# Kernel optimization log

Hardware: AMD Instinct MI355X
Metric: run time of the kernel (lower is better)

Reference implementation:

```python
import jax, jax.numpy as jnp
import numpy as np

B, L, D_MODEL = 2, 2048, 1024
D_INNER, D_STATE, DT_RANK, D_CONV = 2048, 16, 64, 4
EPS = 1e-5


def setup_inputs() -> dict:
    key = jax.random.key(0)
    ks = jax.random.split(key, 12)
    s = lambda fan: 1.0 / np.sqrt(fan)
    return {
        "x": jax.random.normal(ks[0], (B, L, D_MODEL), jnp.float32),
        "norm_w": jnp.ones((D_MODEL,), jnp.float32),
        "W_in": jax.random.normal(ks[1], (2 * D_INNER, D_MODEL), jnp.float32) * s(D_MODEL),
        "W_conv": jax.random.normal(ks[2], (D_INNER, D_CONV), jnp.float32) * s(D_CONV),
        "b_conv": jnp.zeros((D_INNER,), jnp.float32),
        "W_xproj": jax.random.normal(ks[3], (DT_RANK + 2 * D_STATE, D_INNER), jnp.float32) * s(D_INNER),
        "W_dt": jax.random.normal(ks[4], (D_INNER, DT_RANK), jnp.float32) * s(DT_RANK),
        "b_dt": jax.random.normal(ks[5], (D_INNER,), jnp.float32) * 0.1,
        # A initialized as log(1..d_state) per channel (standard Mamba S4D-real init)
        "A_log": jnp.log(jnp.broadcast_to(jnp.arange(1, D_STATE + 1, dtype=jnp.float32), (D_INNER, D_STATE))),
        "D": jnp.ones((D_INNER,), jnp.float32),
        "W_out": jax.random.normal(ks[6], (D_MODEL, D_INNER), jnp.float32) * s(D_INNER),
    }


def _mamba_residual(x, norm_w, W_in, W_conv, b_conv, W_xproj, W_dt, b_dt, A_log, D, W_out):
    # RMSNorm
    xn = x * jax.lax.rsqrt(jnp.mean(x * x, axis=-1, keepdims=True) + EPS) * norm_w
    # in_proj -> split into u (ssm branch) and z (gate)
    xz = jnp.einsum("bld,ed->ble", xn, W_in)            # [b, l, 2*d_inner]
    u, z = jnp.split(xz, 2, axis=-1)                     # each [b, l, d_inner]
    # depthwise causal conv1d over time
    u_t = jnp.transpose(u, (0, 2, 1))                    # [b, d_inner, l]
    u_c = jax.lax.conv_general_dilated(
        u_t, W_conv[:, None, :], window_strides=(1,),
        padding=[(D_CONV - 1, 0)], feature_group_count=D_INNER,
        dimension_numbers=("NCH", "OIH", "NCH"))
    u_c = jax.nn.silu(u_c + b_conv[None, :, None])       # [b, d_inner, l]
    u = jnp.transpose(u_c, (0, 2, 1))                    # [b, l, d_inner]
    # x_proj -> (dt, B, C)
    x_dbl = jnp.einsum("bld,ed->ble", u, W_xproj)        # [b, l, dt_rank+2n]
    dt, Bm, Cm = jnp.split(x_dbl, [DT_RANK, DT_RANK + D_STATE], axis=-1)
    dt = jax.nn.softplus(jnp.einsum("blr,dr->bld", dt, W_dt) + b_dt)  # [b, l, d_inner]
    A = -jnp.exp(A_log)                                  # [d_inner, n]

    # selective scan over time
    def step(h, ins):
        dt_t, B_t, C_t, u_t = ins                        # [b,d],[b,n],[b,n],[b,d]
        dA = jnp.exp(dt_t[..., None] * A)                # [b, d, n]
        h = dA * h + (dt_t * u_t)[..., None] * B_t[:, None, :]
        y = jnp.einsum("bdn,bn->bd", h, C_t)
        return h, y

    h0 = jnp.zeros((x.shape[0], D_INNER, D_STATE), x.dtype)
    ins = (jnp.transpose(dt, (1, 0, 2)), jnp.transpose(Bm, (1, 0, 2)),
           jnp.transpose(Cm, (1, 0, 2)), jnp.transpose(u, (1, 0, 2)))
    _, ys = jax.lax.scan(step, h0, ins)                  # [l, b, d_inner]
    y = jnp.transpose(ys, (1, 0, 2)) + u * D             # [b, l, d_inner]
    y = y * jax.nn.silu(z)
    out = jnp.einsum("ble,de->bld", y, W_out)
    return out + x  # residual (block_mode 'residual'/'none')


def reference(x, norm_w, W_in, W_conv, b_conv, W_xproj, W_dt, b_dt, A_log, D, W_out):
    return _mamba_residual(x, norm_w, W_in, W_conv, b_conv, W_xproj, W_dt, b_dt, A_log, D, W_out)
```

## Files before the change

kernel.cpp:

```cpp
#include <hip/hip_runtime.h>

typedef unsigned short u16;
typedef unsigned int u32;
typedef short bf16x8 __attribute__((ext_vector_type(8)));
typedef float f32x4 __attribute__((ext_vector_type(4)));

static constexpr int LS = 2048;
static constexpr int DM = 1024;
static constexpr int DI = 2048;
static constexpr int DSn = 16;
static constexpr int DTRk = 64;
static constexpr int MR = 4096;
static constexpr int NCH = 64;
static constexpr int CL = LS / NCH;
static constexpr float L2E = 1.44269504f;

#define DEV __device__ __forceinline__

DEV u16 f2bf(float f) {
  u32 u = __float_as_uint(f);
  u32 r = (u + 0x7FFF + ((u >> 16) & 1)) >> 16;
  return (u16)r;
}
DEV float bf2f(u16 h) { return __uint_as_float(((u32)h) << 16); }

DEV void gload16(const u16* g, u16* l) {
  __builtin_amdgcn_global_load_lds((const __attribute__((address_space(1))) u32*)g,
                                   (__attribute__((address_space(3))) u32*)l, 16, 0, 0);
}

DEV void bar() { asm volatile("s_barrier" ::: "memory"); }
DEV void wait_lgkm0() {
  asm volatile("s_waitcnt lgkmcnt(0)" ::: "memory");
  __builtin_amdgcn_sched_barrier(0);
}

#define CALC_POWERS(dst, basev)                                              \
  do {                                                                       \
    const float e1_ = (basev);                                               \
    const float e2_ = e1_ * e1_, e3_ = e2_ * e1_, e4_ = e2_ * e2_;           \
    const float e5_ = e4_ * e1_, e6_ = e4_ * e2_, e7_ = e4_ * e3_,           \
                e8_ = e4_ * e4_;                                             \
    dst[0] = e1_; dst[1] = e2_; dst[2] = e3_; dst[3] = e4_;                  \
    dst[4] = e5_; dst[5] = e6_; dst[6] = e7_; dst[7] = e8_;                  \
    dst[8] = e8_ * e1_;  dst[9] = e8_ * e2_;  dst[10] = e8_ * e3_;           \
    dst[11] = e8_ * e4_; dst[12] = e8_ * e5_; dst[13] = e8_ * e6_;           \
    dst[14] = e8_ * e7_; dst[15] = e8_ * e8_;                                \
  } while (0)

__global__ __launch_bounds__(256) void cvt_weights(const float* __restrict__ W_in,
                                                   const float* __restrict__ W_out,
                                                   const float* __restrict__ W_dt,
                                                   const float* __restrict__ W_xp,
                                                   u16* __restrict__ Win_b,
                                                   u16* __restrict__ Wout_b,
                                                   u16* __restrict__ Wdt_b,
                                                   u16* __restrict__ Wxp_b) {
  const int N0 = 4096 * 1024;
  const int N1 = N0 + 1024 * 2048;
  const int N2 = N1 + 2048 * 64;
  const int N3 = N2 + 128 * 2048;
  int i = blockIdx.x * 256 + threadIdx.x;
  const int stride = gridDim.x * 256;
  for (; i < N3; i += stride) {
    if (i < N0) {
      Win_b[i] = f2bf(W_in[i]);
    } else if (i < N1) {
      const int j = i - N0; Wout_b[j] = f2bf(W_out[j]);
    } else if (i < N2) {
      const int j = i - N1; Wdt_b[j] = f2bf(W_dt[j]);
    } else {
      const int j = i - N2; const int r = j >> 11, c = j & 2047;
      Wxp_b[j] = (r < 96) ? f2bf(W_xp[r * 2048 + c]) : (u16)0;
    }
  }
}

__global__ __launch_bounds__(256) void rmsnorm_kernel(const float* __restrict__ x,
                                                      const float* __restrict__ w,
                                                      u16* __restrict__ xn) {
  const int row = blockIdx.x;
  const int tid = threadIdx.x;
  const float4 v = reinterpret_cast<const float4*>(x + (size_t)row * DM)[tid];
  float ss = v.x * v.x + v.y * v.y + v.z * v.z + v.w * v.w;
#pragma unroll
  for (int o = 32; o; o >>= 1) ss += __shfl_xor(ss, o);
  __shared__ float red[4];
  if ((tid & 63) == 0) red[tid >> 6] = ss;
  __syncthreads();
  const float tot = red[0] + red[1] + red[2] + red[3];
  const float scale = rsqrtf(tot * (1.0f / DM) + 1e-5f);
  const float4 wv = reinterpret_cast<const float4*>(w)[tid];
  ushort4 o4;
  o4.x = f2bf(v.x * scale * wv.x);
  o4.y = f2bf(v.y * scale * wv.y);
  o4.z = f2bf(v.z * scale * wv.z);
  o4.w = f2bf(v.w * scale * wv.w);
  *reinterpret_cast<ushort4*>(&xn[(size_t)row * DM + tid * 4]) = o4;
}

DEV void stage_op(const u16* __restrict__ P, int K, int rowbase, int k0,
                  u16* dst, int tid) {
#pragma unroll
  for (int i = 0; i < 4; ++i) {
    const int row = i * 64 + (tid >> 3);
    const int slot = (tid & 7) ^ (row & 7);
    gload16(P + (size_t)(rowbase + row) * K + k0 + slot * 8, dst + i * 4096 + tid * 8);
  }
}

#define LOAD_A(MH) do { \
  _Pragma("unroll") for (int m_ = 0; m_ < 4; ++m_) \
  _Pragma("unroll") for (int kk_ = 0; kk_ < 2; ++kk_) \
    a[m_][kk_] = *reinterpret_cast<const bf16x8*>( \
        &Asl[curo + wr * 8192 + ((MH) * 64 + m_ * 16 + lrow) * 64 + ((kk_ * 4 + kq) ^ rsw) * 8]); \
} while (0)

#define LOAD_B(NH) do { \
  _Pragma("unroll") for (int n_ = 0; n_ < 2; ++n_) \
  _Pragma("unroll") for (int kk_ = 0; kk_ < 2; ++kk_) \
    b[(NH) * 2 + n_][kk_] = *reinterpret_cast<const bf16x8*>( \
        &Bsl[curo + bh * 8192 + (bq * 64 + ((NH) * 2 + n_) * 16 + lrow) * 64 + ((kk_ * 4 + kq) ^ rsw) * 8]); \
} while (0)

#define MMA_QUAD(MH, NH) do { \
  _Pragma("unroll") for (int m_ = 0; m_ < 4; ++m_) \
  _Pragma("unroll") for (int n_ = 0; n_ < 2; ++n_) \
  _Pragma("unroll") for (int kk_ = 0; kk_ < 2; ++kk_) \
    acc[(MH) * 4 + m_][(NH) * 2 + n_] = __builtin_amdgcn_mfma_f32_16x16x32_bf16( \
        a[m_][kk_], b[(NH) * 2 + n_][kk_], acc[(MH) * 4 + m_][(NH) * 2 + n_], 0, 0, 0); \
} while (0)

__global__ __launch_bounds__(512, 2) void gemm256_bf16(const u16* __restrict__ A,
                                                       const u16* __restrict__ Bw,
                                                       int M, int N, int K,
                                                       u16* __restrict__ outB) {
  __shared__ __align__(16) u16 Asl[2 * 16384];
  __shared__ __align__(16) u16 Bsl[2 * 16384];
  const int tid = threadIdx.x;
  const int lane = tid & 63;
  const int wid = tid >> 6;
  const int wr = wid >> 2;
  const int wc = wid & 3;
  const int lrow = lane & 15;
  const int kq = lane >> 4;
  const int rsw = lane & 7;
  const int bh = wc >> 1, bq = wc & 1;

  const int nwg = gridDim.x * gridDim.y;
  int wg = blockIdx.y * gridDim.x + blockIdx.x;
  wg = (wg & 7) * (nwg >> 3) + (wg >> 3);
  const int bn = (wg % gridDim.x) * 256;
  const int bm = (wg / gridDim.x) * 256;

  const int nt = K >> 6;

  f32x4 acc[8][4] = {};
  bf16x8 a[4][2], b[4][2];

  stage_op(A, K, bm, 0, &Asl[0], tid);
  stage_op(Bw, K, bn, 0, &Bsl[0], tid);
  stage_op(A, K, bm, 64, &Asl[16384], tid);
  stage_op(Bw, K, bn, 64, &Bsl[16384], tid);
  asm volatile("s_waitcnt vmcnt(8)" ::: "memory");
  __builtin_amdgcn_sched_barrier(0);
  bar();

  for (int t = 0; t < nt; ++t) {
    const int curo = (t & 1) * 16384;
    LOAD_A(0); LOAD_B(0);
    bar(); wait_lgkm0();
    __builtin_amdgcn_s_setprio(1); MMA_QUAD(0, 0); __builtin_amdgcn_s_setprio(0);
    bar();
    LOAD_B(1);
    bar(); wait_lgkm0();
    __builtin_amdgcn_s_setprio(1); MMA_QUAD(0, 1); __builtin_amdgcn_s_setprio(0);
    bar();
    LOAD_A(1);
    if (t < nt - 2) stage_op(Bw, K, bn, (t + 2) * 64, &Bsl[curo], tid);
    bar(); wait_lgkm0();
    __builtin_amdgcn_s_setprio(1); MMA_QUAD(1, 0); __builtin_amdgcn_s_setprio(0);
    bar();
    if (t < nt - 2) stage_op(A, K, bm, (t + 2) * 64, &Asl[curo], tid);
    bar();
    __builtin_amdgcn_s_setprio(1); MMA_QUAD(1, 1); __builtin_amdgcn_s_setprio(0);
    if (t == nt - 2) { asm volatile("s_waitcnt vmcnt(0)" ::: "memory"); }
    else if (t < nt - 2) { asm volatile("s_waitcnt vmcnt(6)" ::: "memory"); }
    bar();
  }

#pragma unroll
  for (int m = 0; m < 8; ++m)
#pragma unroll
    for (int n = 0; n < 4; ++n) {
      const int col = bn + wc * 64 + n * 16 + lrow;
#pragma unroll
      for (int rr = 0; rr < 4; ++rr) {
        const int row = bm + wr * 128 + m * 16 + kq * 4 + rr;
        outB[(size_t)row * N + col] = f2bf(acc[m][n][rr]);
      }
    }
}

template <int EPI>
__global__ __launch_bounds__(256) void gemm_bt(const u16* __restrict__ A,
                                               const u16* __restrict__ Bw,
                                               int M, int N, int K, int Klen,
                                               float* __restrict__ outF,
                                               u16* __restrict__ outB,
                                               const float* __restrict__ aux) {
  __shared__ __align__(16) u16 As[128 * 32];
  __shared__ __align__(16) u16 Bs[128 * 32];
  const int tid = threadIdx.x;
  const int lane = tid & 63;
  const int wid = tid >> 6;
  const int wr = wid >> 1, wc = wid & 1;
  const int nwg = gridDim.x * gridDim.y;
  int wg = blockIdx.y * gridDim.x + blockIdx.x;
  wg = (wg & 7) * (nwg >> 3) + (wg >> 3);
  const int bn = (wg % gridDim.x) * 128;
  const int bm = (wg / gridDim.x) * 128;
  const int koff = blockIdx.z * Klen;
  const int r0 = tid >> 2;
  const int c0 = (tid & 3) * 8;
  const int lrow = lane & 15, kq = lane >> 4;

  f32x4 acc[4][4] = {};

  const u16* Ab = A + (size_t)bm * K + koff;
  const u16* Bb = Bw + (size_t)bn * K + koff;

  for (int k0 = 0; k0 < Klen; k0 += 32) {
    gload16(Ab + (size_t)r0 * K + k0 + c0, &As[r0 * 32 + c0]);
    gload16(Ab + (size_t)(r0 + 64) * K + k0 + c0, &As[(r0 + 64) * 32 + c0]);
    gload16(Bb + (size_t)r0 * K + k0 + c0, &Bs[r0 * 32 + c0]);
    gload16(Bb + (size_t)(r0 + 64) * K + k0 + c0, &Bs[(r0 + 64) * 32 + c0]);
    __syncthreads();
    bf16x8 af[4], bfr[4];
#pragma unroll
    for (int m = 0; m < 4; ++m)
      af[m] = *reinterpret_cast<const bf16x8*>(&As[(wr * 64 + m * 16 + lrow) * 32 + kq * 8]);
#pragma unroll
    for (int n = 0; n < 4; ++n)
      bfr[n] = *reinterpret_cast<const bf16x8*>(&Bs[(wc * 64 + n * 16 + lrow) * 32 + kq * 8]);
#pragma unroll
    for (int m = 0; m < 4; ++m)
#pragma unroll
      for (int n = 0; n < 4; ++n)
        acc[m][n] = __builtin_amdgcn_mfma_f32_16x16x32_bf16(af[m], bfr[n], acc[m][n], 0, 0, 0);
    __syncthreads();
  }

  float* dstF = (EPI == 4) ? outF + (size_t)blockIdx.z * MR * N : outF;
#pragma unroll
  for (int m = 0; m < 4; ++m) {
#pragma unroll
    for (int n = 0; n < 4; ++n) {
      const int col = bn + wc * 64 + n * 16 + lrow;
#pragma unroll
      for (int r = 0; r < 4; ++r) {
        const int row = bm + wr * 64 + m * 16 + kq * 4 + r;
        const float v = acc[m][n][r];
        if (EPI == 2) {
          const float xv = v + aux[col];
          const float sp = fmaxf(xv, 0.f) + log1pf(__expf(-fabsf(xv)));
          outB[(size_t)row * N + col] = f2bf(sp);
        } else {
          dstF[(size_t)row * N + col] = v;
        }
      }
    }
  }
}

__global__ __launch_bounds__(256) void outproj_reduce(const float* __restrict__ p,
                                                      const float* __restrict__ x,
                                                      float* __restrict__ out) {
  const int id = blockIdx.x * 256 + threadIdx.x;
  const float4 a = reinterpret_cast<const float4*>(p)[id];
  const float4 b = reinterpret_cast<const float4*>(p + (size_t)MR * 1024)[id];
  const float4 c = reinterpret_cast<const float4*>(x)[id];
  float4 o;
  o.x = a.x + b.x + c.x;
  o.y = a.y + b.y + c.y;
  o.z = a.z + b.z + c.z;
  o.w = a.w + b.w + c.w;
  reinterpret_cast<float4*>(out)[id] = o;
}

__global__ __launch_bounds__(256) void gemm_xproj_splitk(const u16* __restrict__ A,
                                                         const u16* __restrict__ Bw,
                                                         float* __restrict__ p0,
                                                         float* __restrict__ p1) {
  __shared__ __align__(16) u16 As[128 * 32];
  __shared__ __align__(16) u16 Bs[128 * 32];
  const int tid = threadIdx.x;
  const int lane = tid & 63;
  const int wid = tid >> 6;
  const int wr = wid >> 1, wc = wid & 1;
  const int kp = blockIdx.x;
  const int bm = blockIdx.y * 128;
  const int koff = kp * 256;
  const int r0 = tid >> 2;
  const int c0 = (tid & 3) * 8;
  const int lrow = lane & 15, kq = lane >> 4;

  f32x4 acc[4][4] = {};
  const u16* Ab = A + (size_t)bm * DI + koff;
  const u16* Bb = Bw + koff;

  for (int k0 = 0; k0 < 256; k0 += 32) {
    gload16(Ab + (size_t)r0 * DI + k0 + c0, &As[r0 * 32 + c0]);
    gload16(Ab + (size_t)(r0 + 64) * DI + k0 + c0, &As[(r0 + 64) * 32 + c0]);
    gload16(Bb + (size_t)r0 * DI + k0 + c0, &Bs[r0 * 32 + c0]);
    gload16(Bb + (size_t)(r0 + 64) * DI + k0 + c0, &Bs[(r0 + 64) * 32 + c0]);
    __syncthreads();
    bf16x8 af[4], bfr[4];
#pragma unroll
    for (int m = 0; m < 4; ++m)
      af[m] = *reinterpret_cast<const bf16x8*>(&As[(wr * 64 + m * 16 + lrow) * 32 + kq * 8]);
#pragma unroll
    for (int n = 0; n < 4; ++n)
      bfr[n] = *reinterpret_cast<const bf16x8*>(&Bs[(wc * 64 + n * 16 + lrow) * 32 + kq * 8]);
#pragma unroll
    for (int m = 0; m < 4; ++m)
#pragma unroll
      for (int n = 0; n < 4; ++n)
        acc[m][n] = __builtin_amdgcn_mfma_f32_16x16x32_bf16(af[m], bfr[n], acc[m][n], 0, 0, 0);
    __syncthreads();
  }

  float* dst = (kp < 4 ? p0 : p1) + (size_t)(kp & 3) * MR * 128;
#pragma unroll
  for (int m = 0; m < 4; ++m)
#pragma unroll
    for (int n = 0; n < 4; ++n) {
      const int col = wc * 64 + n * 16 + lrow;
#pragma unroll
      for (int r = 0; r < 4; ++r) {
        const int row = bm + wr * 64 + m * 16 + kq * 4 + r;
        dst[(size_t)row * 128 + col] = acc[m][n][r];
      }
    }
}

__global__ __launch_bounds__(256) void xproj_reduce(const float* __restrict__ p0,
                                                    const float* __restrict__ p1,
                                                    float* __restrict__ xdbl,
                                                    u16* __restrict__ dtr) {
  const int id = blockIdx.x * 256 + threadIdx.x;
  const int row = id >> 7, col = id & 127;
  float s = 0.f;
#pragma unroll
  for (int kp = 0; kp < 4; ++kp) s += p0[(size_t)kp * MR * 128 + id];
#pragma unroll
  for (int kp = 0; kp < 4; ++kp) s += p1[(size_t)kp * MR * 128 + id];
  if (col < 96) xdbl[(size_t)row * 96 + col] = s;
  if (col < 64) dtr[(size_t)row * 64 + col] = f2bf(s);
}

__global__ __launch_bounds__(256) void conv_silu_kernel(const u16* __restrict__ xz,
                                                        const float* __restrict__ Wc,
                                                        const float* __restrict__ bc,
                                                        u16* __restrict__ uc) {
  const int id = blockIdx.x * 256 + threadIdx.x;
  const int d8 = id & (DI / 8 - 1);
  const int t = (id >> 8) & (LS - 1);
  const int b = id >> 19;
  const int d0 = d8 * 8;
  const size_t rowb = (size_t)b * LS;
  bf16x8 r[4];
#pragma unroll
  for (int k = 0; k < 4; ++k) {
    const int tt = t - 3 + k;
    if (tt >= 0)
      r[k] = *reinterpret_cast<const bf16x8*>(&xz[(rowb + tt) * (2 * DI) + d0]);
    else
      r[k] = bf16x8{0, 0, 0, 0, 0, 0, 0, 0};
  }
  const float4 bc0 = *reinterpret_cast<const float4*>(&bc[d0]);
  const float4 bc1 = *reinterpret_cast<const float4*>(&bc[d0 + 4]);
  const float bcv[8] = {bc0.x, bc0.y, bc0.z, bc0.w, bc1.x, bc1.y, bc1.z, bc1.w};
  u16 o[8];
#pragma unroll
  for (int j = 0; j < 8; ++j) {
    const float4 w = *reinterpret_cast<const float4*>(&Wc[(d0 + j) * 4]);
    float s = bcv[j];
    s += bf2f((u16)r[0][j]) * w.x;
    s += bf2f((u16)r[1][j]) * w.y;
    s += bf2f((u16)r[2][j]) * w.z;
    s += bf2f((u16)r[3][j]) * w.w;
    const float sl = s / (1.f + __expf(-s));
    o[j] = f2bf(sl);
  }
  *reinterpret_cast<bf16x8*>(&uc[(rowb + t) * DI + d0]) =
      *reinterpret_cast<const bf16x8*>(o);
}


__global__ __launch_bounds__(128, 4) void scan_phase1(const u16* __restrict__ dtb,
                                                      const float* __restrict__ xdbl,
                                                      const u16* __restrict__ uc,
                                                      const float* __restrict__ Alog,
                                                      float* __restrict__ P,
                                                      float* __restrict__ S) {
  __shared__ __align__(16) u16 s_dt[16 * 128];
  __shared__ __align__(16) u16 s_uc[16 * 128];
  __shared__ __align__(16) float s_b[16 * 16];
  const int tid = threadIdx.x;
  const int blk = blockIdx.x;
  const int d0 = (blk & 15) * 128;
  const int c = (blk >> 4) & (NCH - 1);
  const int b = blk >> 10;
  const int d = d0 + tid;
  const size_t tbase = (size_t)b * LS + c * CL;

  float Av[16];
  bool fastA = true;
#pragma unroll
  for (int j = 0; j < 16; j += 4) {
    const float4 Alv = *reinterpret_cast<const float4*>(&Alog[d * DSn + j]);
    Av[j + 0] = -__expf(Alv.x); Av[j + 1] = -__expf(Alv.y);
    Av[j + 2] = -__expf(Alv.z); Av[j + 3] = -__expf(Alv.w);
  }
#pragma unroll
  for (int j = 0; j < 16; ++j)
    fastA = fastA && (fabsf(Av[j] + (float)(j + 1)) < 1e-3f * (float)(j + 1));

  float h[16];
#pragma unroll
  for (int j = 0; j < 16; ++j) h[j] = 0.f;
  float sdt = 0.f;

  for (int w = 0; w < 2; ++w) {
    const size_t twb = tbase + w * 16;
#pragma unroll
    for (int j = 0; j < 2; ++j) {
      const int k = j * 128 + tid;
      const int row = k >> 4, col = (k & 15) * 8;
      gload16(dtb + (twb + row) * DI + d0 + col, &s_dt[row * 128 + col]);
      gload16(uc + (twb + row) * DI + d0 + col, &s_uc[row * 128 + col]);
    }
    if (tid < 64) {
      gload16((const u16*)(xdbl + (twb + (tid >> 2)) * 96 + DTRk + (tid & 3) * 4),
              (u16*)&s_b[tid * 4]);
    }
    __syncthreads();
    if (fastA) {
      for (int tr = 0; tr < 16; ++tr) {
        const float dtv = bf2f(s_dt[tr * 128 + tid]);
        const float uv = bf2f(s_uc[tr * 128 + tid]);
        const float du = dtv * uv;
        sdt += dtv;
        float dA[16];
        CALC_POWERS(dA, exp2f(-L2E * dtv));
        float Bf[16];
#pragma unroll
        for (int j = 0; j < 16; j += 4) {
          const float4 Bv = *reinterpret_cast<const float4*>(&s_b[tr * 16 + j]);
          Bf[j] = Bv.x; Bf[j + 1] = Bv.y; Bf[j + 2] = Bv.z; Bf[j + 3] = Bv.w;
        }
#pragma unroll
        for (int j = 0; j < 16; ++j) h[j] = dA[j] * h[j] + du * Bf[j];
      }
    } else {
      for (int tr = 0; tr < 16; ++tr) {
        const float dtv = bf2f(s_dt[tr * 128 + tid]);
        const float uv = bf2f(s_uc[tr * 128 + tid]);
        const float du = dtv * uv;
        sdt += dtv;
        float Bf[16];
#pragma unroll
        for (int j = 0; j < 16; j += 4) {
          const float4 Bv = *reinterpret_cast<const float4*>(&s_b[tr * 16 + j]);
          Bf[j] = Bv.x; Bf[j + 1] = Bv.y; Bf[j + 2] = Bv.z; Bf[j + 3] = Bv.w;
        }
#pragma unroll
        for (int j = 0; j < 16; ++j)
          h[j] = exp2f(dtv * Av[j] * L2E) * h[j] + du * Bf[j];
      }
    }
    __syncthreads();
  }

  const size_t oi = (((size_t)b * NCH + c) * DI + d) * DSn;
  float Pw[16];
  if (fastA) {
    CALC_POWERS(Pw, exp2f(-L2E * sdt));
  } else {
#pragma unroll
    for (int j = 0; j < 16; ++j) Pw[j] = exp2f(Av[j] * L2E * sdt);
  }
#pragma unroll
  for (int j = 0; j < 16; j += 4) {
    float4 Sv = {h[j], h[j + 1], h[j + 2], h[j + 3]};
    float4 Pv = {Pw[j], Pw[j + 1], Pw[j + 2], Pw[j + 3]};
    *reinterpret_cast<float4*>(&S[oi + j]) = Sv;
    *reinterpret_cast<float4*>(&P[oi + j]) = Pv;
  }
}

__global__ __launch_bounds__(256) void scan_phase2(const float* __restrict__ P,
                                                   float* __restrict__ S) {
  const int gid = blockIdx.x * 256 + threadIdx.x;
  const int ng = gid & 3;
  const int d = (gid >> 2) & (DI - 1);
  const int b = gid >> 13;
  float4 h = {0.f, 0.f, 0.f, 0.f};
  for (int cc = 0; cc < NCH; ++cc) {
    const size_t oi = (((size_t)b * NCH + cc) * DI + d) * DSn + ng * 4;
    const float4 Pv = *reinterpret_cast<const float4*>(&P[oi]);
    const float4 Sv = *reinterpret_cast<const float4*>(&S[oi]);
    *reinterpret_cast<float4*>(&S[oi]) = h;
    h.x = Sv.x + Pv.x * h.x;
    h.y = Sv.y + Pv.y * h.y;
    h.z = Sv.z + Pv.z * h.z;
    h.w = Sv.w + Pv.w * h.w;
  }
}

__global__ __launch_bounds__(128, 4) void scan_phase3(const u16* __restrict__ dtb,
                                                      const float* __restrict__ xdbl,
                                                      const u16* __restrict__ uc,
                                                      const u16* __restrict__ xz,
                                                      const float* __restrict__ Alog,
                                                      const float* __restrict__ Dp,
                                                      const float* __restrict__ Hin,
                                                      u16* __restrict__ yb) {
  __shared__ __align__(16) u16 s_dt[16 * 128];
  __shared__ __align__(16) u16 s_uc[16 * 128];
  __shared__ __align__(16) u16 s_z[16 * 128];
  __shared__ __align__(16) float s_bc[16 * 32];
  const int tid = threadIdx.x;
  const int blk = blockIdx.x;
  const int d0 = (blk & 15) * 128;
  const int c = (blk >> 4) & (NCH - 1);
  const int b = blk >> 10;
  const int d = d0 + tid;
  const size_t tbase = (size_t)b * LS + c * CL;

  float Av[16];
  bool fastA = true;
#pragma unroll
  for (int j = 0; j < 16; j += 4) {
    const float4 Alv = *reinterpret_cast<const float4*>(&Alog[d * DSn + j]);
    Av[j + 0] = -__expf(Alv.x); Av[j + 1] = -__expf(Alv.y);
    Av[j + 2] = -__expf(Alv.z); Av[j + 3] = -__expf(Alv.w);
  }
#pragma unroll
  for (int j = 0; j < 16; ++j)
    fastA = fastA && (fabsf(Av[j] + (float)(j + 1)) < 1e-3f * (float)(j + 1));

  const float Dd = Dp[d];
  const size_t oi = (((size_t)b * NCH + c) * DI + d) * DSn;
  float h[16];
#pragma unroll
  for (int j = 0; j < 16; j += 4) {
    const float4 hv = *reinterpret_cast<const float4*>(&Hin[oi + j]);
    h[j] = hv.x; h[j + 1] = hv.y; h[j + 2] = hv.z; h[j + 3] = hv.w;
  }

  for (int w = 0; w < 2; ++w) {
    const size_t twb = tbase + w * 16;
#pragma unroll
    for (int j = 0; j < 2; ++j) {
      const int k = j * 128 + tid;
      const int row = k >> 4, col = (k & 15) * 8;
      gload16(dtb + (twb + row) * DI + d0 + col, &s_dt[row * 128 + col]);
      gload16(uc + (twb + row) * DI + d0 + col, &s_uc[row * 128 + col]);
      gload16(xz + (twb + row) * (2 * DI) + DI + d0 + col, &s_z[row * 128 + col]);
    }
    {
      gload16((const u16*)(xdbl + (twb + (tid >> 3)) * 96 + DTRk + (tid & 7) * 4),
              (u16*)&s_bc[tid * 4]);
    }
    __syncthreads();
#define P3_STEP(DA_STMT)                                                        \
    for (int tr = 0; tr < 16; ++tr) {                                           \
      const float dtv = bf2f(s_dt[tr * 128 + tid]);                             \
      const float uv = bf2f(s_uc[tr * 128 + tid]);                              \
      const float du = dtv * uv;                                                \
      float dA[16];                                                             \
      DA_STMT;                                                                  \
      float Bf[16], Cf[16];                                                     \
      _Pragma("unroll")                                                         \
      for (int j = 0; j < 16; j += 4) {                                         \
        const float4 Bv = *reinterpret_cast<const float4*>(&s_bc[tr * 32 + j]); \
        const float4 Cv = *reinterpret_cast<const float4*>(&s_bc[tr * 32 + 16 + j]); \
        Bf[j] = Bv.x; Bf[j + 1] = Bv.y; Bf[j + 2] = Bv.z; Bf[j + 3] = Bv.w;     \
        Cf[j] = Cv.x; Cf[j + 1] = Cv.y; Cf[j + 2] = Cv.z; Cf[j + 3] = Cv.w;     \
      }                                                                         \
      _Pragma("unroll")                                                         \
      for (int j = 0; j < 16; ++j) h[j] = dA[j] * h[j] + du * Bf[j];            \
      float y0 = 0.f, y1 = 0.f, y2 = 0.f, y3 = 0.f;                             \
      _Pragma("unroll")                                                         \
      for (int j = 0; j < 16; j += 4) {                                         \
        y0 += h[j] * Cf[j];                                                     \
        y1 += h[j + 1] * Cf[j + 1];                                             \
        y2 += h[j + 2] * Cf[j + 2];                                             \
        y3 += h[j + 3] * Cf[j + 3];                                             \
      }                                                                         \
      const float y = (y0 + y1) + (y2 + y3) + uv * Dd;                          \
      const float z = bf2f(s_z[tr * 128 + tid]);                                \
      const float sz = z / (1.f + __expf(-z));                                  \
      yb[(twb + tr) * DI + d] = f2bf(y * sz);                                   \
    }
    if (fastA) {
      P3_STEP(CALC_POWERS(dA, exp2f(-L2E * dtv)));
    } else {
      P3_STEP({ _Pragma("unroll") for (int j = 0; j < 16; ++j) dA[j] = exp2f(dtv * Av[j] * L2E); });
    }
#undef P3_STEP
    __syncthreads();
  }
}

extern "C" void kernel_launch(void* const* d_in, const int* in_sizes, int n_in,
                              void* d_out, int out_size, void* d_ws, size_t ws_size,
                              hipStream_t stream) {
  (void)in_sizes; (void)n_in; (void)out_size; (void)ws_size;
  const float* x      = (const float*)d_in[0];
  const float* norm_w = (const float*)d_in[1];
  const float* W_in   = (const float*)d_in[2];
  const float* W_conv = (const float*)d_in[3];
  const float* b_conv = (const float*)d_in[4];
  const float* W_xp   = (const float*)d_in[5];
  const float* W_dt   = (const float*)d_in[6];
  const float* b_dt   = (const float*)d_in[7];
  const float* A_log  = (const float*)d_in[8];
  const float* Dvec   = (const float*)d_in[9];
  const float* W_out  = (const float*)d_in[10];
  float* out = (float*)d_out;

  char* ws = (char*)d_ws;
  size_t off = 0;
  auto alloc = [&](size_t bytes) -> void* {
    void* p = ws + off;
    off += (bytes + 255) & ~(size_t)255;
    return p;
  };
  u16* Win_b  = (u16*)alloc((size_t)4096 * 1024 * 2);
  u16* Wout_b = (u16*)alloc((size_t)1024 * 2048 * 2);
  u16* Wxp_b  = (u16*)alloc((size_t)128 * 2048 * 2);
  u16* Wdt_b  = (u16*)alloc((size_t)2048 * 64 * 2);
  u16* xn_b   = (u16*)alloc((size_t)MR * DM * 2);
  u16* xz_b   = (u16*)alloc((size_t)MR * 2 * DI * 2);
  u16* uc_b   = (u16*)alloc((size_t)MR * DI * 2);
  float* xdbl = (float*)alloc((size_t)MR * 96 * 4);
  u16* dtr_b  = (u16*)alloc((size_t)MR * 64 * 2);
  u16* dtf_b  = (u16*)alloc((size_t)MR * DI * 2);
  u16* y_b    = (u16*)alloc((size_t)MR * DI * 2);
  float* Sbuf = (float*)alloc((size_t)2 * NCH * DI * DSn * 4);
  float* part0 = (float*)Win_b;
  float* part1 = (float*)xn_b;
  float* Pbuf = (float*)y_b;
  float* opart = (float*)xz_b;

  cvt_weights<<<2048, 256, 0, stream>>>(W_in, W_out, W_dt, W_xp,
                                        Win_b, Wout_b, Wdt_b, Wxp_b);

  rmsnorm_kernel<<<MR, 256, 0, stream>>>(x, norm_w, xn_b);

  gemm256_bf16<<<dim3(16, 16), 512, 0, stream>>>(xn_b, Win_b, MR, 4096, 1024, xz_b);
  conv_silu_kernel<<<4096, 256, 0, stream>>>(xz_b, W_conv, b_conv, uc_b);
  gemm_xproj_splitk<<<dim3(8, 32), 256, 0, stream>>>(uc_b, Wxp_b, part0, part1);
  xproj_reduce<<<2048, 256, 0, stream>>>(part0, part1, xdbl, dtr_b);
  gemm_bt<2><<<dim3(16, 32), 256, 0, stream>>>(dtr_b, Wdt_b, MR, 2048, 64, 64,
                                               nullptr, dtf_b, b_dt);
  scan_phase1<<<2048, 128, 0, stream>>>(dtf_b, xdbl, uc_b, A_log, Pbuf, Sbuf);
  scan_phase2<<<64, 256, 0, stream>>>(Pbuf, Sbuf);
  scan_phase3<<<2048, 128, 0, stream>>>(dtf_b, xdbl, uc_b, xz_b, A_log, Dvec,
                                        Sbuf, y_b);
  gemm_bt<4><<<dim3(8, 32, 2), 256, 0, stream>>>(y_b, Wout_b, MR, 1024, 2048, 1024,
                                                 opart, nullptr, nullptr);
  outproj_reduce<<<4096, 256, 0, stream>>>(opart, x, out);
}
```

Baseline: 231.3 us.

## Run out-projection on pipelined 256x256 GEMM with 4-way split-K

```diff
diff --git a/kernel.cpp b/kernel.cpp
--- a/kernel.cpp
+++ b/kernel.cpp
@@ -131,10 +131,12 @@
         a[m_][kk_], b[(NH) * 2 + n_][kk_], acc[(MH) * 4 + m_][(NH) * 2 + n_], 0, 0, 0); \
 } while (0)
 
-__global__ __launch_bounds__(512, 2) void gemm256_bf16(const u16* __restrict__ A,
-                                                       const u16* __restrict__ Bw,
-                                                       int M, int N, int K,
-                                                       u16* __restrict__ outB) {
+template <int EPI>
+__global__ __launch_bounds__(512, 2) void gemm256(const u16* __restrict__ A,
+                                                  const u16* __restrict__ Bw,
+                                                  int M, int N, int K, int Klen,
+                                                  u16* __restrict__ outB,
+                                                  float* __restrict__ outF) {
   __shared__ __align__(16) u16 Asl[2 * 16384];
   __shared__ __align__(16) u16 Bsl[2 * 16384];
   const int tid = threadIdx.x;
@@ -152,16 +154,17 @@
   wg = (wg & 7) * (nwg >> 3) + (wg >> 3);
   const int bn = (wg % gridDim.x) * 256;
   const int bm = (wg / gridDim.x) * 256;
-
-  const int nt = K >> 6;
+  const int koff = blockIdx.z * Klen;
+
+  const int nt = Klen >> 6;
 
   f32x4 acc[8][4] = {};
   bf16x8 a[4][2], b[4][2];
 
-  stage_op(A, K, bm, 0, &Asl[0], tid);
-  stage_op(Bw, K, bn, 0, &Bsl[0], tid);
-  stage_op(A, K, bm, 64, &Asl[16384], tid);
-  stage_op(Bw, K, bn, 64, &Bsl[16384], tid);
+  stage_op(A, K, bm, koff, &Asl[0], tid);
+  stage_op(Bw, K, bn, koff, &Bsl[0], tid);
+  stage_op(A, K, bm, koff + 64, &Asl[16384], tid);
+  stage_op(Bw, K, bn, koff + 64, &Bsl[16384], tid);
   asm volatile("s_waitcnt vmcnt(8)" ::: "memory");
   __builtin_amdgcn_sched_barrier(0);
   bar();
@@ -177,36 +180,62 @@
     __builtin_amdgcn_s_setprio(1); MMA_QUAD(0, 1); __builtin_amdgcn_s_setprio(0);
     bar();
     LOAD_A(1);
-    if (t < nt - 2) stage_op(Bw, K, bn, (t + 2) * 64, &Bsl[curo], tid);
+    if (t < nt - 2) stage_op(Bw, K, bn, koff + (t + 2) * 64, &Bsl[curo], tid);
     bar(); wait_lgkm0();
     __builtin_amdgcn_s_setprio(1); MMA_QUAD(1, 0); __builtin_amdgcn_s_setprio(0);
     bar();
-    if (t < nt - 2) stage_op(A, K, bm, (t + 2) * 64, &Asl[curo], tid);
+    if (t < nt - 2) stage_op(A, K, bm, koff + (t + 2) * 64, &Asl[curo], tid);
     bar();
     __builtin_amdgcn_s_setprio(1); MMA_QUAD(1, 1); __builtin_amdgcn_s_setprio(0);
     if (t == nt - 2) { asm volatile("s_waitcnt vmcnt(0)" ::: "memory"); }
-    else if (t < nt - 2) { asm volatile("s_waitcnt vmcnt(6)" ::: "memory"); }
+    else if (t < nt - 2) { asm volatile("s_waitcnt vmcnt(8)" ::: "memory"); }
     bar();
   }
 
-#pragma unroll
-  for (int m = 0; m < 8; ++m)
-#pragma unroll
-    for (int n = 0; n < 4; ++n) {
-      const int col = bn + wc * 64 + n * 16 + lrow;
-#pragma unroll
-      for (int rr = 0; rr < 4; ++rr) {
-        const int row = bm + wr * 128 + m * 16 + kq * 4 + rr;
-        outB[(size_t)row * N + col] = f2bf(acc[m][n][rr]);
+  if (EPI == 0) {
+#pragma unroll
+    for (int m = 0; m < 8; ++m)
+#pragma unroll
+      for (int n = 0; n < 4; ++n) {
+        const int col = bn + wc * 64 + n * 16 + lrow;
+#pragma unroll
+        for (int rr = 0; rr < 4; ++rr) {
+          const int row = bm + wr * 128 + m * 16 + kq * 4 + rr;
+          outB[(size_t)row * N + col] = f2bf(acc[m][n][rr]);
+        }
       }
-    }
-}
-
-template <int EPI>
-__global__ __launch_bounds__(256) void gemm_bt(const u16* __restrict__ A,
+  } else {
+    float* dstF = outF + (size_t)blockIdx.z * MR * N;
+#pragma unroll
+    for (int m = 0; m < 8; ++m)
+#pragma unroll
+      for (int n = 0; n < 4; ++n) {
+        const int col = bn + wc * 64 + n * 16 + lrow;
+#pragma unroll
+        for (int rr = 0; rr < 4; ++rr) {
+          const int row = bm + wr * 128 + m * 16 + kq * 4 + rr;
+          dstF[(size_t)row * N + col] = acc[m][n][rr];
+        }
+      }
+  }
+}
+
+__global__ __launch_bounds__(256) void outproj_reduce4(const float* __restrict__ p,
+                                                       const float* __restrict__ x,
+                                                       float* __restrict__ out) {
+  const int id = blockIdx.x * 256 + threadIdx.x;
+  float4 o = reinterpret_cast<const float4*>(x)[id];
+#pragma unroll
+  for (int s = 0; s < 4; ++s) {
+    const float4 a = reinterpret_cast<const float4*>(p + (size_t)s * MR * 1024)[id];
+    o.x += a.x; o.y += a.y; o.z += a.z; o.w += a.w;
+  }
+  reinterpret_cast<float4*>(out)[id] = o;
+}
+
+__global__ __launch_bounds__(256) void gemm_dt(const u16* __restrict__ A,
                                                const u16* __restrict__ Bw,
-                                               int M, int N, int K, int Klen,
-                                               float* __restrict__ outF,
+                                               int M, int N, int K,
                                                u16* __restrict__ outB,
                                                const float* __restrict__ aux) {
   __shared__ __align__(16) u16 As[128 * 32];
@@ -220,17 +249,16 @@
   wg = (wg & 7) * (nwg >> 3) + (wg >> 3);
   const int bn = (wg % gridDim.x) * 128;
   const int bm = (wg / gridDim.x) * 128;
-  const int koff = blockIdx.z * Klen;
   const int r0 = tid >> 2;
   const int c0 = (tid & 3) * 8;
   const int lrow = lane & 15, kq = lane >> 4;
 
   f32x4 acc[4][4] = {};
 
-  const u16* Ab = A + (size_t)bm * K + koff;
-  const u16* Bb = Bw + (size_t)bn * K + koff;
-
-  for (int k0 = 0; k0 < Klen; k0 += 32) {
+  const u16* Ab = A + (size_t)bm * K;
+  const u16* Bb = Bw + (size_t)bn * K;
+
+  for (int k0 = 0; k0 < K; k0 += 32) {
     gload16(Ab + (size_t)r0 * K + k0 + c0, &As[r0 * 32 + c0]);
     gload16(Ab + (size_t)(r0 + 64) * K + k0 + c0, &As[(r0 + 64) * 32 + c0]);
     gload16(Bb + (size_t)r0 * K + k0 + c0, &Bs[r0 * 32 + c0]);
@@ -251,7 +279,6 @@
     __syncthreads();
   }
 
-  float* dstF = (EPI == 4) ? outF + (size_t)blockIdx.z * MR * N : outF;
 #pragma unroll
   for (int m = 0; m < 4; ++m) {
 #pragma unroll
@@ -260,32 +287,12 @@
 #pragma unroll
       for (int r = 0; r < 4; ++r) {
         const int row = bm + wr * 64 + m * 16 + kq * 4 + r;
-        const float v = acc[m][n][r];
-        if (EPI == 2) {
-          const float xv = v + aux[col];
-          const float sp = fmaxf(xv, 0.f) + log1pf(__expf(-fabsf(xv)));
-          outB[(size_t)row * N + col] = f2bf(sp);
-        } else {
-          dstF[(size_t)row * N + col] = v;
-        }
+        const float xv = acc[m][n][r] + aux[col];
+        const float sp = fmaxf(xv, 0.f) + log1pf(__expf(-fabsf(xv)));
+        outB[(size_t)row * N + col] = f2bf(sp);
       }
     }
   }
-}
-
-__global__ __launch_bounds__(256) void outproj_reduce(const float* __restrict__ p,
-                                                      const float* __restrict__ x,
-                                                      float* __restrict__ out) {
-  const int id = blockIdx.x * 256 + threadIdx.x;
-  const float4 a = reinterpret_cast<const float4*>(p)[id];
-  const float4 b = reinterpret_cast<const float4*>(p + (size_t)MR * 1024)[id];
-  const float4 c = reinterpret_cast<const float4*>(x)[id];
-  float4 o;
-  o.x = a.x + b.x + c.x;
-  o.y = a.y + b.y + c.y;
-  o.z = a.z + b.z + c.z;
-  o.w = a.w + b.w + c.w;
-  reinterpret_cast<float4*>(out)[id] = o;
 }
 
 __global__ __launch_bounds__(256) void gemm_xproj_splitk(const u16* __restrict__ A,
@@ -661,17 +668,17 @@
 
   rmsnorm_kernel<<<MR, 256, 0, stream>>>(x, norm_w, xn_b);
 
-  gemm256_bf16<<<dim3(16, 16), 512, 0, stream>>>(xn_b, Win_b, MR, 4096, 1024, xz_b);
+  gemm256<0><<<dim3(16, 16, 1), 512, 0, stream>>>(xn_b, Win_b, MR, 4096, 1024, 1024,
+                                                  xz_b, nullptr);
   conv_silu_kernel<<<4096, 256, 0, stream>>>(xz_b, W_conv, b_conv, uc_b);
   gemm_xproj_splitk<<<dim3(8, 32), 256, 0, stream>>>(uc_b, Wxp_b, part0, part1);
   xproj_reduce<<<2048, 256, 0, stream>>>(part0, part1, xdbl, dtr_b);
-  gemm_bt<2><<<dim3(16, 32), 256, 0, stream>>>(dtr_b, Wdt_b, MR, 2048, 64, 64,
-                                               nullptr, dtf_b, b_dt);
+  gemm_dt<<<dim3(16, 32), 256, 0, stream>>>(dtr_b, Wdt_b, MR, 2048, 64, dtf_b, b_dt);
   scan_phase1<<<2048, 128, 0, stream>>>(dtf_b, xdbl, uc_b, A_log, Pbuf, Sbuf);
   scan_phase2<<<64, 256, 0, stream>>>(Pbuf, Sbuf);
   scan_phase3<<<2048, 128, 0, stream>>>(dtf_b, xdbl, uc_b, xz_b, A_log, Dvec,
                                         Sbuf, y_b);
-  gemm_bt<4><<<dim3(8, 32, 2), 256, 0, stream>>>(y_b, Wout_b, MR, 1024, 2048, 1024,
-                                                 opart, nullptr, nullptr);
-  outproj_reduce<<<4096, 256, 0, stream>>>(opart, x, out);
-}
+  gemm256<1><<<dim3(4, 16, 4), 512, 0, stream>>>(y_b, Wout_b, MR, 1024, 2048, 512,
+                                                 nullptr, opart);
+  outproj_reduce4<<<4096, 256, 0, stream>>>(opart, x, out);
+}
```

New measurement: 230.1 us. Within noise of the previous version (-0.5%).
